# Kernel tuning notes

Measured on AMD Instinct MI355X. Metric: run time of the kernel, lower is better.

The kernel has to match this reference:

```python
import jax, jax.numpy as jnp
import numpy as np

EPS = 1e-12  # torch F.normalize default eps


def _l2norm(t, axis=-1):
    n = jnp.sqrt(jnp.sum(t * t, axis=axis, keepdims=True))
    return t / jnp.maximum(n, EPS)


def setup_inputs() -> dict:
    key = jax.random.key(0)
    ks = jax.random.split(key, 5)
    B, N, C, H = 8, 4096, 1024, 16
    x = jax.random.normal(ks[0], (B, N, C), dtype=jnp.float32)
    # nn.Linear(dim, 3*dim, bias=False): weight [3C, C]; we store transposed [C, 3C]
    w_qkv = jax.random.normal(ks[1], (C, 3 * C), dtype=jnp.float32) * (1.0 / np.sqrt(C))
    temperature = jnp.ones((H, 1, 1), dtype=jnp.float32)
    w_proj = jax.random.normal(ks[2], (C, C), dtype=jnp.float32) * (1.0 / np.sqrt(C))
    b_proj = jax.random.normal(ks[3], (C,), dtype=jnp.float32) * 0.01
    return {"x": x, "w_qkv": w_qkv, "temperature": temperature,
            "w_proj": w_proj, "b_proj": b_proj}


def reference(x, w_qkv, temperature, w_proj, b_proj):
    B, N, C = x.shape
    H = temperature.shape[0]
    dh = C // H
    # qkv: [B, N, 3C] -> [B, N, 3, H, dh] -> q/k/v each [B, H, dh, N]
    qkv = (x @ w_qkv).reshape(B, N, 3, H, dh).transpose(2, 0, 3, 4, 1)
    q, k, v = qkv[0], qkv[1], qkv[2]
    # L2-normalize over token axis (last dim)
    q = _l2norm(q)
    k = _l2norm(k)
    # channel-channel attention: [B, H, dh, dh]
    attn = jnp.einsum("bhdn,bhen->bhde", q, k) * temperature  # temp broadcasts [H,1,1]
    attn = jax.nn.softmax(attn, axis=-1)
    # weighted sum over channels: [B, H, dh, N] -> [B, N, C]
    out = jnp.einsum("bhde,bhen->bhdn", attn, v).transpose(0, 3, 1, 2).reshape(B, N, C)
    return out @ w_proj + b_proj
```

## Files before the change

kernel.cpp:

```cpp
#include <hip/hip_runtime.h>
#include <cstdint>

typedef unsigned short u16;
typedef unsigned int u32;
typedef __attribute__((ext_vector_type(8))) short bf16x8;
typedef __attribute__((ext_vector_type(4))) float f32x4;

typedef const u32 __attribute__((address_space(1)))* gp_t;
typedef u32 __attribute__((address_space(3)))* lp_t;

__device__ __forceinline__ u16 f2bf(float f) {
    union { float f; u32 u; } v; v.f = f;
    u32 r = v.u + 0x7FFFu + ((v.u >> 16) & 1u);
    return (u16)(r >> 16);
}
__device__ __forceinline__ float bf2f(u16 h) {
    union { u32 u; float f; } v; v.u = ((u32)h) << 16;
    return v.f;
}

__global__ __launch_bounds__(256) void k_pack2(const float* __restrict__ x,
                                               u16* __restrict__ xt, u16* __restrict__ xc) {
    __shared__ u16 tb[64][72];
    const int blk = blockIdx.x;
    const int tt = blk >> 4, ct = blk & 15;
    const long tok0 = (long)tt * 64;
    const int ch0 = ct * 64;
    const int tid = threadIdx.x;
    const int row = tid >> 2, cq = tid & 3;
#pragma unroll
    for (int jj = 0; jj < 4; ++jj) {
        const float4 v = *(const float4*)(x + (tok0 + row) * 1024 + ch0 + cq * 16 + jj * 4);
        tb[row][cq * 16 + jj * 4 + 0] = f2bf(v.x);
        tb[row][cq * 16 + jj * 4 + 1] = f2bf(v.y);
        tb[row][cq * 16 + jj * 4 + 2] = f2bf(v.z);
        tb[row][cq * 16 + jj * 4 + 3] = f2bf(v.w);
    }
    __syncthreads();
#pragma unroll
    for (int s = 0; s < 2; ++s) {
        const int c = s * 256 + tid;
        const int r2 = c >> 3, col8 = c & 7;
        *(uint4*)(xt + (tok0 + r2) * 1024 + ch0 + col8 * 8) = *(const uint4*)(&tb[r2][col8 * 8]);
    }
    const int b = (int)(tok0 >> 12);
    const int nin = (int)(tok0 & 4095);
#pragma unroll
    for (int s = 0; s < 2; ++s) {
        const int c = s * 256 + tid;
        const int crow = c >> 3, t8 = c & 7;
        u16 u[8];
#pragma unroll
        for (int k = 0; k < 8; ++k) u[k] = tb[t8 * 8 + k][crow];
        *(uint4*)(xc + ((long)b * 1024 + ch0 + crow) * 4096 + nin + t8 * 8) = *(const uint4*)u;
    }
}

__global__ __launch_bounds__(256) void k_prep(
    const float* __restrict__ wqkv, const float* __restrict__ wproj,
    u16* __restrict__ wqT, u16* __restrict__ wpT, u16* __restrict__ wvb)
{
    __shared__ float t[64][65];
    const int blk = blockIdx.x;
    const int tid = threadIdx.x;
    if (blk < 1024) {
        const float* src; u16* dst; int ncols, lb;
        if (blk < 768) { src = wqkv; dst = wqT; ncols = 3072; lb = blk; }
        else           { src = wproj; dst = wpT; ncols = 1024; lb = blk - 768; }
        const int ntn = ncols >> 6;
        const int kb = (lb / ntn) * 64;
        const int nb = (lb % ntn) * 64;
        for (int i = tid; i < 4096; i += 256) {
            int r = i >> 6, c = i & 63;
            t[r][c] = src[(long)(kb + r) * ncols + nb + c];
        }
        __syncthreads();
        for (int i = tid; i < 4096; i += 256) {
            int r = i >> 6, c = i & 63;
            dst[(long)(nb + r) * 1024 + kb + c] = f2bf(t[c][r]);
        }
    } else {
        const int idx = (blk - 1024) * 256 + tid;
        const int cin = idx >> 7, e0 = (idx & 127) * 8;
        const float4 v1 = *(const float4*)(wqkv + (long)cin * 3072 + 2048 + e0);
        const float4 v2 = *(const float4*)(wqkv + (long)cin * 3072 + 2048 + e0 + 4);
        u16 u[8];
        u[0] = f2bf(v1.x); u[1] = f2bf(v1.y); u[2] = f2bf(v1.z); u[3] = f2bf(v1.w);
        u[4] = f2bf(v2.x); u[5] = f2bf(v2.y); u[6] = f2bf(v2.z); u[7] = f2bf(v2.w);
        *(uint4*)(wvb + (long)cin * 1024 + e0) = *(const uint4*)u;
    }
}

__global__ __launch_bounds__(256) void k_g128p(
    const u16* __restrict__ xc, float* __restrict__ Sp)
{
    __shared__ u16 sm[8192];

    const int tid = threadIdx.x;
    const int wid = tid >> 6, lane = tid & 63;
    const int wr = wid >> 1, wc = wid & 1;
    const int fr = lane & 15, sl = lane >> 4;

    const int nwg = gridDim.x;
    const int logical = (blockIdx.x & 7) * (nwg >> 3) + (blockIdx.x >> 3);
    const int kseg = logical & 3;
    const int bt = logical >> 2;
    const int b = bt / 36;
    int t = bt % 36;
    int i0 = 0;
    while (t >= 8 - i0) { t -= 8 - i0; ++i0; }
    const int j0 = i0 + t;
    const int m0 = i0 * 128, n0 = j0 * 128;

    const u16* base = xc + (long)b * 4194304 + kseg * 1024;

    const int srow = lane >> 2;
    const int sslot = lane & 3;

    f32x4 acc[4][4];
#pragma unroll
    for (int i = 0; i < 4; ++i)
#pragma unroll
        for (int j = 0; j < 4; ++j) acc[i][j] = (f32x4){0.f, 0.f, 0.f, 0.f};

    for (int kt = 0; kt < 1024; kt += 32) {
        __syncthreads();
#pragma unroll
        for (int i = 0; i < 2; ++i) {
            const int row = wid * 32 + i * 16 + srow;
            const int swz = (sslot ^ ((row >> 1) & 3)) << 3;
            const u16* ga = base + (long)(m0 + row) * 4096 + kt + swz;
            const u16* gb = base + (long)(n0 + row) * 4096 + kt + swz;
            __builtin_amdgcn_global_load_lds((gp_t)ga, (lp_t)(sm + (wid * 2 + i) * 512), 16, 0, 0);
            __builtin_amdgcn_global_load_lds((gp_t)gb, (lp_t)(sm + 4096 + (wid * 2 + i) * 512), 16, 0, 0);
        }
        __syncthreads();
        bf16x8 af[4], bfr[4];
#pragma unroll
        for (int mi = 0; mi < 4; ++mi) {
            const int row = wr * 64 + mi * 16 + fr;
            af[mi] = *(const bf16x8*)(sm + row * 32 + ((sl ^ ((row >> 1) & 3)) << 3));
        }
#pragma unroll
        for (int ni = 0; ni < 4; ++ni) {
            const int row = wc * 64 + ni * 16 + fr;
            bfr[ni] = *(const bf16x8*)(sm + 4096 + row * 32 + ((sl ^ ((row >> 1) & 3)) << 3));
        }
#pragma unroll
        for (int mi = 0; mi < 4; ++mi)
#pragma unroll
            for (int ni = 0; ni < 4; ++ni)
                acc[mi][ni] = __builtin_amdgcn_mfma_f32_16x16x32_bf16(af[mi], bfr[ni], acc[mi][ni], 0, 0, 0);
    }

    float* gp = Sp + (long)logical * 16384;
#pragma unroll
    for (int mi = 0; mi < 4; ++mi)
#pragma unroll
        for (int ni = 0; ni < 4; ++ni)
#pragma unroll
            for (int rr = 0; rr < 4; ++rr)
                gp[(wr * 64 + mi * 16 + sl * 4 + rr) * 128 + wc * 64 + ni * 16 + fr] = acc[mi][ni][rr];
}

__global__ __launch_bounds__(256) void k_sred(const float* __restrict__ Sp, u16* __restrict__ S)
{
    __shared__ u16 lC[128 * 136];
    __shared__ u16 lCT[128 * 136];

    const int tid = threadIdx.x;
    const int nwg = gridDim.x;
    const int logical = (blockIdx.x & 7) * (nwg >> 3) + (blockIdx.x >> 3);
    const int b = logical / 36;
    int t = logical % 36;
    int i0 = 0;
    while (t >= 8 - i0) { t -= 8 - i0; ++i0; }
    const int j0 = i0 + t;
    const int m0 = i0 * 128, n0 = j0 * 128;

    const float* p = Sp + (long)logical * 65536;
    for (int i = tid; i < 16384; i += 256) {
        const float s = p[i] + p[i + 16384] + p[i + 32768] + p[i + 49152];
        const u16 v = f2bf(s);
        const int r_ = i >> 7, c_ = i & 127;
        lC[r_ * 136 + c_] = v;
        lCT[c_ * 136 + r_] = v;
    }
    __syncthreads();
    const int tk = tid >> 1, half = tid & 1;
    {
        u16* dp = S + (long)b * 1048576 + (long)(m0 + tk) * 1024 + n0 + half * 64;
        const u16* sp1 = lC + tk * 136 + half * 64;
#pragma unroll
        for (int i = 0; i < 8; ++i) ((uint4*)dp)[i] = ((const uint4*)sp1)[i];
    }
    if (i0 != j0) {
        u16* dp = S + (long)b * 1048576 + (long)(n0 + tk) * 1024 + m0 + half * 64;
        const u16* sp2 = lCT + tk * 136 + half * 64;
#pragma unroll
        for (int i = 0; i < 8; ++i) ((uint4*)dp)[i] = ((const uint4*)sp2)[i];
    }
}

__global__ __launch_bounds__(256) void k_g128(
    const u16* __restrict__ A, long Ab, const u16* __restrict__ Bt, long Bs,
    u16* __restrict__ C, long Cb, int K, int MT, int NT)
{
    __shared__ u16 sm[8192];
    __shared__ u16 lC[128 * 136];

    const int tid = threadIdx.x;
    const int wid = tid >> 6, lane = tid & 63;
    const int wr = wid >> 1, wc = wid & 1;
    const int fr = lane & 15, sl = lane >> 4;

    const int nwg = gridDim.x;
    const int logical = (blockIdx.x & 7) * (nwg >> 3) + (blockIdx.x >> 3);

    const int b = logical / (MT * NT);
    const int r = logical % (MT * NT);
    const int i0 = r / NT, j0 = r % NT;
    const int m0 = i0 * 128, n0 = j0 * 128;
    const u16* Abp = A + (long)b * Ab;
    const u16* Bbp = Bt + (long)b * Bs;
    u16* Cbp = C + (long)b * Cb;

    const int srow = lane >> 2;
    const int sslot = lane & 3;

    f32x4 acc[4][4];
#pragma unroll
    for (int i = 0; i < 4; ++i)
#pragma unroll
        for (int j = 0; j < 4; ++j) acc[i][j] = (f32x4){0.f, 0.f, 0.f, 0.f};

    for (int kt = 0; kt < K; kt += 32) {
        __syncthreads();
#pragma unroll
        for (int i = 0; i < 2; ++i) {
            const int row = wid * 32 + i * 16 + srow;
            const int swz = (sslot ^ ((row >> 1) & 3)) << 3;
            const u16* ga = Abp + (long)(m0 + row) * K + kt + swz;
            const u16* gb = Bbp + (long)(n0 + row) * K + kt + swz;
            __builtin_amdgcn_global_load_lds((gp_t)ga, (lp_t)(sm + (wid * 2 + i) * 512), 16, 0, 0);
            __builtin_amdgcn_global_load_lds((gp_t)gb, (lp_t)(sm + 4096 + (wid * 2 + i) * 512), 16, 0, 0);
        }
        __syncthreads();
        bf16x8 af[4], bfr[4];
#pragma unroll
        for (int mi = 0; mi < 4; ++mi) {
            const int row = wr * 64 + mi * 16 + fr;
            af[mi] = *(const bf16x8*)(sm + row * 32 + ((sl ^ ((row >> 1) & 3)) << 3));
        }
#pragma unroll
        for (int ni = 0; ni < 4; ++ni) {
            const int row = wc * 64 + ni * 16 + fr;
            bfr[ni] = *(const bf16x8*)(sm + 4096 + row * 32 + ((sl ^ ((row >> 1) & 3)) << 3));
        }
#pragma unroll
        for (int mi = 0; mi < 4; ++mi)
#pragma unroll
            for (int ni = 0; ni < 4; ++ni)
                acc[mi][ni] = __builtin_amdgcn_mfma_f32_16x16x32_bf16(af[mi], bfr[ni], acc[mi][ni], 0, 0, 0);
    }
    __syncthreads();

#pragma unroll
    for (int mi = 0; mi < 4; ++mi)
#pragma unroll
        for (int ni = 0; ni < 4; ++ni) {
            const int ch = wc * 64 + ni * 16 + fr;
            const int tk = wr * 64 + mi * 16 + sl * 4;
#pragma unroll
            for (int rr = 0; rr < 4; ++rr)
                lC[(tk + rr) * 136 + ch] = f2bf(acc[mi][ni][rr]);
        }
    __syncthreads();
    {
        const int tk = tid >> 1, half = tid & 1;
        const u16* sp = lC + tk * 136 + half * 64;
        u16* dp = Cbp + (long)(m0 + tk) * 1024 + n0 + half * 64;
#pragma unroll
        for (int i = 0; i < 8; ++i) ((uint4*)dp)[i] = ((const uint4*)sp)[i];
    }
}

template<int EPI>
__global__ __launch_bounds__(512, 2) void k_gemm256(
    const u16* __restrict__ A, long Ab, const u16* __restrict__ Bt, long Bs,
    int MT, int NT,
    u16* __restrict__ cB, float* __restrict__ cF, long Cb, const float* __restrict__ bias)
{
    __shared__ uint4 smem4[8704];
    u16* sm = (u16*)smem4;

    const int tid = threadIdx.x;
    const int wid = tid >> 6, lane = tid & 63;
    const int wr = wid >> 2, wc = wid & 3;
    const int fr = lane & 15, sl = lane >> 4;

    const int nwg = gridDim.x;
    const int logical = (blockIdx.x & 7) * (nwg >> 3) + (blockIdx.x >> 3);
    const int b = logical / (MT * NT);
    const int rem = logical % (MT * NT);
    const int mt = rem / NT, nt = rem % NT;
    const long m0 = (long)mt * 256;
    const int n0 = nt * 256;

    const int srow = wid * 32 + (lane >> 2);
    const int kswz = (((lane & 3) ^ ((srow >> 1) & 3)) << 3);
    const u16* gA = A + (long)b * Ab + (m0 + srow) * 1024L + kswz;
    const u16* gB = Bt + (long)b * Bs + ((long)n0 + srow) * 1024L + kswz;
    const int ldst = wid * 1024;

    const int fxor = ((sl ^ ((fr >> 1) & 3)) << 3);
    const int aBase = (wr * 128 + fr) * 32 + fxor;
    const int bBase = 32768 + (wc * 64 + fr) * 32 + fxor;

    f32x4 acc[8][4];
#pragma unroll
    for (int i = 0; i < 8; ++i)
#pragma unroll
        for (int j = 0; j < 4; ++j) acc[i][j] = (f32x4){0.f, 0.f, 0.f, 0.f};

#define STAGE_A(d, kh, ts) do { \
    const u16* g_ = gA + (ts) * 64 + (kh) * 32; \
    u16* l_ = sm + (d) * 16384 + (kh) * 8192 + ldst; \
    __builtin_amdgcn_global_load_lds((gp_t)g_, (lp_t)l_, 16, 0, 0); \
    __builtin_amdgcn_global_load_lds((gp_t)(g_ + 16 * 1024), (lp_t)(l_ + 512), 16, 0, 0); \
} while (0)
#define STAGE_B(d, kh, ts) do { \
    const u16* g_ = gB + (ts) * 64 + (kh) * 32; \
    u16* l_ = sm + 32768 + (d) * 16384 + (kh) * 8192 + ldst; \
    __builtin_amdgcn_global_load_lds((gp_t)g_, (lp_t)l_, 16, 0, 0); \
    __builtin_amdgcn_global_load_lds((gp_t)(g_ + 16 * 1024), (lp_t)(l_ + 512), 16, 0, 0); \
} while (0)

    STAGE_A(0, 0, 0); STAGE_B(0, 0, 0);
    STAGE_A(0, 1, 0); STAGE_B(0, 1, 0);
    STAGE_A(1, 0, 1); STAGE_B(1, 0, 1);
    asm volatile("s_waitcnt vmcnt(8)" ::: "memory");
    __builtin_amdgcn_s_barrier();

    bf16x8 afX[4], afY[4], bfX[4], bfY[4];
#pragma unroll
    for (int ni = 0; ni < 4; ++ni) bfX[ni] = *(const bf16x8*)(sm + bBase + ni * 512);
#pragma unroll
    for (int mi = 0; mi < 4; ++mi) afX[mi] = *(const bf16x8*)(sm + aBase + mi * 512);

#pragma unroll 2
    for (int T = 0; T < 16; ++T) {
        const int d = T & 1;
        const int t1 = (T + 1 < 16) ? T + 1 : 15;
        const int t2 = (T + 2 < 16) ? T + 2 : 15;
        const int base = d * 16384;
        const int nbase = (d ^ 1) * 16384;

#pragma unroll
        for (int mi = 0; mi < 4; ++mi)
            afY[mi] = *(const bf16x8*)(sm + aBase + (4 + mi) * 512 + base);
        STAGE_A(d ^ 1, 1, t1);
        asm volatile("s_waitcnt vmcnt(6)" ::: "memory");
        __builtin_amdgcn_s_barrier();
        __builtin_amdgcn_s_setprio(1);
#pragma unroll
        for (int mi = 0; mi < 4; ++mi)
#pragma unroll
            for (int ni = 0; ni < 4; ++ni)
                acc[mi][ni] = __builtin_amdgcn_mfma_f32_16x16x32_bf16(afX[mi], bfX[ni], acc[mi][ni], 0, 0, 0);
        __builtin_amdgcn_s_setprio(0);
        __builtin_amdgcn_s_barrier();

#pragma unroll
        for (int ni = 0; ni < 4; ++ni)
            bfY[ni] = *(const bf16x8*)(sm + bBase + ni * 512 + base + 8192);
#pragma unroll
        for (int mi = 0; mi < 4; ++mi)
            afX[mi] = *(const bf16x8*)(sm + aBase + mi * 512 + base + 8192);
        STAGE_B(d ^ 1, 1, t1);
        __builtin_amdgcn_s_barrier();
        __builtin_amdgcn_s_setprio(1);
#pragma unroll
        for (int mi = 0; mi < 4; ++mi)
#pragma unroll
            for (int ni = 0; ni < 4; ++ni)
                acc[mi + 4][ni] = __builtin_amdgcn_mfma_f32_16x16x32_bf16(afY[mi], bfX[ni], acc[mi + 4][ni], 0, 0, 0);
        __builtin_amdgcn_s_setprio(0);
        __builtin_amdgcn_s_barrier();

#pragma unroll
        for (int mi = 0; mi < 4; ++mi)
            afY[mi] = *(const bf16x8*)(sm + aBase + (4 + mi) * 512 + base + 8192);
        STAGE_A(d, 0, t2);
        asm volatile("s_waitcnt vmcnt(6)" ::: "memory");
        __builtin_amdgcn_s_barrier();
        __builtin_amdgcn_s_setprio(1);
#pragma unroll
        for (int mi = 0; mi < 4; ++mi)
#pragma unroll
            for (int ni = 0; ni < 4; ++ni)
                acc[mi][ni] = __builtin_amdgcn_mfma_f32_16x16x32_bf16(afX[mi], bfY[ni], acc[mi][ni], 0, 0, 0);
        __builtin_amdgcn_s_setprio(0);
        __builtin_amdgcn_s_barrier();

#pragma unroll
        for (int ni = 0; ni < 4; ++ni)
            bfX[ni] = *(const bf16x8*)(sm + bBase + ni * 512 + nbase);
#pragma unroll
        for (int mi = 0; mi < 4; ++mi)
            afX[mi] = *(const bf16x8*)(sm + aBase + mi * 512 + nbase);
        STAGE_B(d, 0, t2);
        __builtin_amdgcn_s_barrier();
        __builtin_amdgcn_s_setprio(1);
#pragma unroll
        for (int mi = 0; mi < 4; ++mi)
#pragma unroll
            for (int ni = 0; ni < 4; ++ni)
                acc[mi + 4][ni] = __builtin_amdgcn_mfma_f32_16x16x32_bf16(afY[mi], bfY[ni], acc[mi + 4][ni], 0, 0, 0);
        __builtin_amdgcn_s_setprio(0);
        __builtin_amdgcn_s_barrier();
    }
#undef STAGE_A
#undef STAGE_B
    asm volatile("s_waitcnt vmcnt(0)" ::: "memory");
    __syncthreads();

    if (EPI == 0) {
        u16* cbase = cB + (long)b * Cb;
        u16* piece = sm + wid * 8704;
#pragma unroll
        for (int mi = 0; mi < 8; ++mi)
#pragma unroll
            for (int ni = 0; ni < 4; ++ni) {
                const int ch = ni * 16 + fr;
                const int tk = mi * 16 + sl * 4;
#pragma unroll
                for (int rr = 0; rr < 4; ++rr)
                    piece[(tk + rr) * 68 + ch] = f2bf(acc[mi][ni][rr]);
            }
        __syncthreads();
#pragma unroll
        for (int i = 0; i < 32; ++i) {
            const int chunk = i * 512 + tid;
            const int row = chunk >> 4, c8 = chunk & 15;
            const int p = row >> 7, tk = row & 127;
            const int wrp = p >> 2, wcp = p & 3;
            const uint2 v = *(const uint2*)(sm + p * 8704 + tk * 68 + c8 * 4);
            *(uint2*)(cbase + (m0 + wrp * 128 + tk) * 1024L + n0 + wcp * 64 + c8 * 4) = v;
        }
    } else {
        float* cbase = cF + (long)b * Cb;
        float bi[4];
#pragma unroll
        for (int ni = 0; ni < 4; ++ni) bi[ni] = bias[n0 + wc * 64 + ni * 16 + fr];
#pragma unroll
        for (int pass = 0; pass < 2; ++pass) {
            float* pieceF = (float*)smem4 + wid * 4352;
            if (pass) __syncthreads();
#pragma unroll
            for (int mi2 = 0; mi2 < 4; ++mi2) {
                const int mi = pass * 4 + mi2;
#pragma unroll
                for (int ni = 0; ni < 4; ++ni) {
                    const int ch = ni * 16 + fr;
                    const int tk = mi2 * 16 + sl * 4;
#pragma unroll
                    for (int rr = 0; rr < 4; ++rr)
                        pieceF[(tk + rr) * 68 + ch] = acc[mi][ni][rr] + bi[ni];
                }
            }
            __syncthreads();
#pragma unroll
            for (int i = 0; i < 16; ++i) {
                const int chunk = i * 512 + tid;
                const int row = chunk >> 4, c4 = chunk & 15;
                const int p = row >> 6, tk = row & 63;
                const int wrp = p >> 2, wcp = p & 3;
                const float4 v = *(const float4*)((float*)smem4 + p * 4352 + tk * 68 + c4 * 4);
                *(float4*)(cbase + (m0 + wrp * 128 + pass * 64 + tk) * 1024L + n0 + wcp * 64 + c4 * 4) = v;
            }
        }
    }
}

__global__ __launch_bounds__(256) void k_gram2p(
    const u16* __restrict__ wqT, const u16* __restrict__ Ut,
    float* __restrict__ g2p, float* __restrict__ sq2p)
{
    __shared__ u16 lQ[64 * 256];
    __shared__ u16 lK[64 * 256];

    const int blk = blockIdx.x;
    const int seg = blk & 3, bh = blk >> 2;
    const int b = bh >> 4, h = bh & 15;
    const int tid = threadIdx.x;
    const int wid = tid >> 6, lane = tid & 63;

    {
        const int r2 = lane >> 5, slot = lane & 31;
        const int rbase = wid * 16;
#pragma unroll
        for (int i = 0; i < 8; ++i) {
            const int r = rbase + i * 2 + r2;
            const int col = seg * 256 + ((slot ^ (r & 7)) << 3);
            const u16* gq = wqT + (long)(h * 64 + r) * 1024 + col;
            const u16* gk = Ut + ((long)b * 2048 + 1024 + h * 64 + r) * 1024 + col;
            __builtin_amdgcn_global_load_lds((gp_t)gq, (lp_t)(lQ + (rbase + i * 2) * 256), 16, 0, 0);
            __builtin_amdgcn_global_load_lds((gp_t)gk, (lp_t)(lK + (rbase + i * 2) * 256), 16, 0, 0);
        }
    }
    __syncthreads();

    {
        const int row = tid >> 1, half = tid & 1;
        const int j = (row < 64) ? (h * 64 + row) : (1024 + h * 64 + (row - 64));
        const u16* pa = wqT + (long)j * 1024 + seg * 256 + half * 128;
        const u16* pb = Ut + ((long)b * 2048 + j) * 1024 + seg * 256 + half * 128;
        float s = 0.f;
#pragma unroll 4
        for (int i = 0; i < 16; ++i) {
            const uint4 a = *(const uint4*)(pa + i * 8);
            const uint4 bv = *(const uint4*)(pb + i * 8);
            s += bf2f((u16)(a.x & 0xFFFF)) * bf2f((u16)(bv.x & 0xFFFF));
            s += bf2f((u16)(a.x >> 16))    * bf2f((u16)(bv.x >> 16));
            s += bf2f((u16)(a.y & 0xFFFF)) * bf2f((u16)(bv.y & 0xFFFF));
            s += bf2f((u16)(a.y >> 16))    * bf2f((u16)(bv.y >> 16));
            s += bf2f((u16)(a.z & 0xFFFF)) * bf2f((u16)(bv.z & 0xFFFF));
            s += bf2f((u16)(a.z >> 16))    * bf2f((u16)(bv.z >> 16));
            s += bf2f((u16)(a.w & 0xFFFF)) * bf2f((u16)(bv.w & 0xFFFF));
            s += bf2f((u16)(a.w >> 16))    * bf2f((u16)(bv.w >> 16));
        }
        s += __shfl_xor(s, 1);
        if (half == 0) sq2p[(long)blk * 128 + row] = s;
    }

    const int fr = lane & 15, sl = lane >> 4;
    f32x4 acc[4];
#pragma unroll
    for (int i = 0; i < 4; ++i) acc[i] = (f32x4){0.f, 0.f, 0.f, 0.f};
#pragma unroll
    for (int ks = 0; ks < 8; ++ks) {
        const int ra = wid * 16 + fr;
        const bf16x8 a = *(const bf16x8*)(lQ + ra * 256 + (((ks * 4 + sl) ^ (ra & 7)) << 3));
#pragma unroll
        for (int ni = 0; ni < 4; ++ni) {
            const int rb = ni * 16 + fr;
            const bf16x8 bb = *(const bf16x8*)(lK + rb * 256 + (((ks * 4 + sl) ^ (rb & 7)) << 3));
            acc[ni] = __builtin_amdgcn_mfma_f32_16x16x32_bf16(a, bb, acc[ni], 0, 0, 0);
        }
    }
    float* gp = g2p + (long)blk * 4096;
#pragma unroll
    for (int ni = 0; ni < 4; ++ni)
#pragma unroll
        for (int rr = 0; rr < 4; ++rr)
            gp[(wid * 16 + sl * 4 + rr) * 64 + ni * 16 + fr] = acc[ni][rr];
}

__global__ __launch_bounds__(256) void k_swmix(
    const float* __restrict__ g2p, const float* __restrict__ sq2p,
    const float* __restrict__ temperature,
    const u16* __restrict__ wpT, u16* __restrict__ wmix)
{
    __shared__ u16 lA[64 * 72];
    __shared__ u16 lB[256 * 64];

    const int blk = blockIdx.x;
    const int nseg = blk & 3, bh = blk >> 2;
    const int b = bh >> 4, h = bh & 15;
    const int tid = threadIdx.x;
    const int wid = tid >> 6, lane = tid & 63;
    const int fr = lane & 15, sl = lane >> 4;

#pragma unroll
    for (int i = 0; i < 8; ++i) {
        const int cc = wid * 8 + i;
        const int row = cc * 8 + (lane >> 3);
        const int slot = lane & 7;
        const u16* g = wpT + (long)(nseg * 256 + row) * 1024 + h * 64 + ((slot ^ (row & 7)) << 3);
        __builtin_amdgcn_global_load_lds((gp_t)g, (lp_t)(lB + cc * 512), 16, 0, 0);
    }

    {
        const int e = lane;
        const float* sp = sq2p + (long)bh * 512;
        float sqk = 0.f;
#pragma unroll
        for (int s = 0; s < 4; ++s) sqk += sp[s * 128 + 64 + e];
        const float rk = 1.f / fmaxf(sqrtf(sqk), 1e-12f);
        const float temp = temperature[h];
        const float* gp = g2p + (long)bh * 16384;
#pragma unroll 2
        for (int i = 0; i < 16; ++i) {
            const int d = wid * 16 + i;
            float raw = 0.f, sqq = 0.f;
#pragma unroll
            for (int s = 0; s < 4; ++s) {
                raw += gp[s * 4096 + d * 64 + e];
                sqq += sp[s * 128 + d];
            }
            const float rq = 1.f / fmaxf(sqrtf(sqq), 1e-12f);
            const float v = raw * rq * rk * temp;
            float mx = v;
#pragma unroll
            for (int o = 32; o; o >>= 1) mx = fmaxf(mx, __shfl_xor(mx, o));
            const float p = __expf(v - mx);
            float sum = p;
#pragma unroll
            for (int o = 32; o; o >>= 1) sum += __shfl_xor(sum, o);
            lA[e * 72 + d] = f2bf(p / sum);
        }
    }
    __syncthreads();

    f32x4 acc[4][4];
#pragma unroll
    for (int i = 0; i < 4; ++i)
#pragma unroll
        for (int j = 0; j < 4; ++j) acc[i][j] = (f32x4){0.f, 0.f, 0.f, 0.f};

#pragma unroll
    for (int ks = 0; ks < 2; ++ks) {
        bf16x8 a[4], bb[4];
#pragma unroll
        for (int mi = 0; mi < 4; ++mi)
            a[mi] = *(const bf16x8*)(lA + (mi * 16 + fr) * 72 + ks * 32 + sl * 8);
#pragma unroll
        for (int ni = 0; ni < 4; ++ni) {
            const int rb = wid * 64 + ni * 16 + fr;
            bb[ni] = *(const bf16x8*)(lB + rb * 64 + (((ks * 4 + sl) ^ (rb & 7)) << 3));
        }
#pragma unroll
        for (int mi = 0; mi < 4; ++mi)
#pragma unroll
            for (int ni = 0; ni < 4; ++ni)
                acc[mi][ni] = __builtin_amdgcn_mfma_f32_16x16x32_bf16(a[mi], bb[ni], acc[mi][ni], 0, 0, 0);
    }

    u16* dst = wmix + ((long)b << 20);
#pragma unroll
    for (int mi = 0; mi < 4; ++mi)
#pragma unroll
        for (int ni = 0; ni < 4; ++ni) {
            const int cout = nseg * 256 + wid * 64 + ni * 16 + fr;
            const int e0 = mi * 16 + sl * 4;
            ushort4 w;
            w.x = f2bf(acc[mi][ni][0]); w.y = f2bf(acc[mi][ni][1]);
            w.z = f2bf(acc[mi][ni][2]); w.w = f2bf(acc[mi][ni][3]);
            *(ushort4*)(dst + (long)cout * 1024 + h * 64 + e0) = w;
        }
}

extern "C" void kernel_launch(void* const* d_in, const int* in_sizes, int n_in,
                              void* d_out, int out_size, void* d_ws, size_t ws_size,
                              hipStream_t stream) {
    const float* x = (const float*)d_in[0];
    const float* w_qkv = (const float*)d_in[1];
    const float* temperature = (const float*)d_in[2];
    const float* w_proj = (const float*)d_in[3];
    const float* b_proj = (const float*)d_in[4];
    float* out = (float*)d_out;
    char* ws = (char*)d_ws;

    u16* wqT    = (u16*)(ws);
    u16* wpT    = (u16*)(ws + 6291456);
    u16* wvb    = (u16*)(ws + 8388608);
    u16* xt     = (u16*)(ws + 10485760);
    u16* xc     = (u16*)(ws + 77594624);
    u16* S      = (u16*)(ws + 144703488);
    float* Sp   = (float*)(ws + 161480704);
    u16* Ut     = (u16*)(ws + 161480704);
    float* g2p  = (float*)(ws + 195035136);
    float* sq2p = (float*)(ws + 203423744);
    u16* wmix   = (u16*)(ws + 204734464);
    u16* wfinT  = (u16*)(ws + 221511680);

    k_pack2<<<8192, 256, 0, stream>>>(x, xt, xc);
    k_prep<<<1536, 256, 0, stream>>>(w_qkv, w_proj, wqT, wpT, wvb);
    k_g128p<<<1152, 256, 0, stream>>>(xc, Sp);
    k_sred<<<288, 256, 0, stream>>>(Sp, S);
    k_gemm256<0><<<256, 512, 0, stream>>>(wqT, 0L, S, 1048576L, 8, 4, Ut, nullptr, 2097152L, nullptr);
    k_gram2p<<<512, 256, 0, stream>>>(wqT, Ut, g2p, sq2p);
    k_swmix<<<512, 256, 0, stream>>>(g2p, sq2p, temperature, wpT, wmix);
    k_g128<<<512, 256, 0, stream>>>(wmix, 1048576L, wvb, 0L, wfinT, 1048576L, 1024, 8, 8);
    k_gemm256<1><<<512, 512, 0, stream>>>(xt, 4194304L, wfinT, 1048576L, 16, 4, nullptr, out, 4194304L, b_proj);
}
```

Before: 345.3 us.

## Merge pack and prep kernels, halve Gram split-K, store partials as bf16

The x pack/transposition kernel and the weight prep kernel are merged into one launch with block-range dispatch. The Gram split-K goes from 4 segments to 2 (576 blocks, each doing twice the K loop), and partial results are written as bf16 instead of fp32. The reduction kernel reads the bf16 halves with vectorised loads. This cuts partial-sum traffic and one launch, at the cost of fewer blocks for the Gram GEMM (under-occupancy risk) and extra rounding of the partials.

```diff
diff --git a/kernel.cpp b/kernel.cpp
--- a/kernel.cpp
+++ b/kernel.cpp
@@ -19,68 +19,66 @@
     return v.f;
 }
 
-__global__ __launch_bounds__(256) void k_pack2(const float* __restrict__ x,
-                                               u16* __restrict__ xt, u16* __restrict__ xc) {
-    __shared__ u16 tb[64][72];
-    const int blk = blockIdx.x;
-    const int tt = blk >> 4, ct = blk & 15;
-    const long tok0 = (long)tt * 64;
-    const int ch0 = ct * 64;
-    const int tid = threadIdx.x;
-    const int row = tid >> 2, cq = tid & 3;
-#pragma unroll
-    for (int jj = 0; jj < 4; ++jj) {
-        const float4 v = *(const float4*)(x + (tok0 + row) * 1024 + ch0 + cq * 16 + jj * 4);
-        tb[row][cq * 16 + jj * 4 + 0] = f2bf(v.x);
-        tb[row][cq * 16 + jj * 4 + 1] = f2bf(v.y);
-        tb[row][cq * 16 + jj * 4 + 2] = f2bf(v.z);
-        tb[row][cq * 16 + jj * 4 + 3] = f2bf(v.w);
-    }
-    __syncthreads();
-#pragma unroll
-    for (int s = 0; s < 2; ++s) {
-        const int c = s * 256 + tid;
-        const int r2 = c >> 3, col8 = c & 7;
-        *(uint4*)(xt + (tok0 + r2) * 1024 + ch0 + col8 * 8) = *(const uint4*)(&tb[r2][col8 * 8]);
-    }
-    const int b = (int)(tok0 >> 12);
-    const int nin = (int)(tok0 & 4095);
-#pragma unroll
-    for (int s = 0; s < 2; ++s) {
-        const int c = s * 256 + tid;
-        const int crow = c >> 3, t8 = c & 7;
-        u16 u[8];
-#pragma unroll
-        for (int k = 0; k < 8; ++k) u[k] = tb[t8 * 8 + k][crow];
-        *(uint4*)(xc + ((long)b * 1024 + ch0 + crow) * 4096 + nin + t8 * 8) = *(const uint4*)u;
-    }
-}
-
-__global__ __launch_bounds__(256) void k_prep(
-    const float* __restrict__ wqkv, const float* __restrict__ wproj,
+__global__ __launch_bounds__(256) void k_prepack(
+    const float* __restrict__ x, const float* __restrict__ wqkv, const float* __restrict__ wproj,
+    u16* __restrict__ xt, u16* __restrict__ xc,
     u16* __restrict__ wqT, u16* __restrict__ wpT, u16* __restrict__ wvb)
 {
-    __shared__ float t[64][65];
+    __shared__ float tf[64][65];
     const int blk = blockIdx.x;
     const int tid = threadIdx.x;
-    if (blk < 1024) {
+
+    if (blk < 8192) {
+        u16* tb = (u16*)tf;
+        const int tt = blk >> 4, ct = blk & 15;
+        const long tok0 = (long)tt * 64;
+        const int ch0 = ct * 64;
+        const int row = tid >> 2, cq = tid & 3;
+#pragma unroll
+        for (int jj = 0; jj < 4; ++jj) {
+            const float4 v = *(const float4*)(x + (tok0 + row) * 1024 + ch0 + cq * 16 + jj * 4);
+            tb[row * 72 + cq * 16 + jj * 4 + 0] = f2bf(v.x);
+            tb[row * 72 + cq * 16 + jj * 4 + 1] = f2bf(v.y);
+            tb[row * 72 + cq * 16 + jj * 4 + 2] = f2bf(v.z);
+            tb[row * 72 + cq * 16 + jj * 4 + 3] = f2bf(v.w);
+        }
+        __syncthreads();
+#pragma unroll
+        for (int s = 0; s < 2; ++s) {
+            const int c = s * 256 + tid;
+            const int r2 = c >> 3, col8 = c & 7;
+            *(uint4*)(xt + (tok0 + r2) * 1024 + ch0 + col8 * 8) = *(const uint4*)(&tb[r2 * 72 + col8 * 8]);
+        }
+        const int b = (int)(tok0 >> 12);
+        const int nin = (int)(tok0 & 4095);
+#pragma unroll
+        for (int s = 0; s < 2; ++s) {
+            const int c = s * 256 + tid;
+            const int crow = c >> 3, t8 = c & 7;
+            u16 u[8];
+#pragma unroll
+            for (int k = 0; k < 8; ++k) u[k] = tb[(t8 * 8 + k) * 72 + crow];
+            *(uint4*)(xc + ((long)b * 1024 + ch0 + crow) * 4096 + nin + t8 * 8) = *(const uint4*)u;
+        }
+    } else if (blk < 9216) {
+        const int lb0 = blk - 8192;
         const float* src; u16* dst; int ncols, lb;
-        if (blk < 768) { src = wqkv; dst = wqT; ncols = 3072; lb = blk; }
-        else           { src = wproj; dst = wpT; ncols = 1024; lb = blk - 768; }
+        if (lb0 < 768) { src = wqkv; dst = wqT; ncols = 3072; lb = lb0; }
+        else           { src = wproj; dst = wpT; ncols = 1024; lb = lb0 - 768; }
         const int ntn = ncols >> 6;
         const int kb = (lb / ntn) * 64;
         const int nb = (lb % ntn) * 64;
         for (int i = tid; i < 4096; i += 256) {
             int r = i >> 6, c = i & 63;
-            t[r][c] = src[(long)(kb + r) * ncols + nb + c];
+            tf[r][c] = src[(long)(kb + r) * ncols + nb + c];
         }
         __syncthreads();
         for (int i = tid; i < 4096; i += 256) {
             int r = i >> 6, c = i & 63;
-            dst[(long)(nb + r) * 1024 + kb + c] = f2bf(t[c][r]);
+            dst[(long)(nb + r) * 1024 + kb + c] = f2bf(tf[c][r]);
         }
     } else {
-        const int idx = (blk - 1024) * 256 + tid;
+        const int idx = (blk - 9216) * 256 + tid;
         const int cin = idx >> 7, e0 = (idx & 127) * 8;
         const float4 v1 = *(const float4*)(wqkv + (long)cin * 3072 + 2048 + e0);
         const float4 v2 = *(const float4*)(wqkv + (long)cin * 3072 + 2048 + e0 + 4);
@@ -92,7 +90,7 @@
 }
 
 __global__ __launch_bounds__(256) void k_g128p(
-    const u16* __restrict__ xc, float* __restrict__ Sp)
+    const u16* __restrict__ xc, u16* __restrict__ Spb)
 {
     __shared__ u16 sm[8192];
 
@@ -103,8 +101,8 @@
 
     const int nwg = gridDim.x;
     const int logical = (blockIdx.x & 7) * (nwg >> 3) + (blockIdx.x >> 3);
-    const int kseg = logical & 3;
-    const int bt = logical >> 2;
+    const int kseg = logical & 1;
+    const int bt = logical >> 1;
     const int b = bt / 36;
     int t = bt % 36;
     int i0 = 0;
@@ -112,7 +110,7 @@
     const int j0 = i0 + t;
     const int m0 = i0 * 128, n0 = j0 * 128;
 
-    const u16* base = xc + (long)b * 4194304 + kseg * 1024;
+    const u16* base = xc + (long)b * 4194304 + kseg * 2048;
 
     const int srow = lane >> 2;
     const int sslot = lane & 3;
@@ -123,7 +121,7 @@
 #pragma unroll
         for (int j = 0; j < 4; ++j) acc[i][j] = (f32x4){0.f, 0.f, 0.f, 0.f};
 
-    for (int kt = 0; kt < 1024; kt += 32) {
+    for (int kt = 0; kt < 2048; kt += 32) {
         __syncthreads();
 #pragma unroll
         for (int i = 0; i < 2; ++i) {
@@ -153,17 +151,20 @@
                 acc[mi][ni] = __builtin_amdgcn_mfma_f32_16x16x32_bf16(af[mi], bfr[ni], acc[mi][ni], 0, 0, 0);
     }
 
-    float* gp = Sp + (long)logical * 16384;
+    u16* gp = Spb + (long)logical * 16384;
 #pragma unroll
     for (int mi = 0; mi < 4; ++mi)
 #pragma unroll
-        for (int ni = 0; ni < 4; ++ni)
+        for (int ni = 0; ni < 4; ++ni) {
+            const int rw = wr * 64 + mi * 16 + sl * 4;
+            const int cl = wc * 64 + ni * 16 + fr;
 #pragma unroll
             for (int rr = 0; rr < 4; ++rr)
-                gp[(wr * 64 + mi * 16 + sl * 4 + rr) * 128 + wc * 64 + ni * 16 + fr] = acc[mi][ni][rr];
-}
-
-__global__ __launch_bounds__(256) void k_sred(const float* __restrict__ Sp, u16* __restrict__ S)
+                gp[(rw + rr) * 128 + cl] = f2bf(acc[mi][ni][rr]);
+        }
+}
+
+__global__ __launch_bounds__(256) void k_sred(const u16* __restrict__ Spb, u16* __restrict__ S)
 {
     __shared__ u16 lC[128 * 136];
     __shared__ u16 lCT[128 * 136];
@@ -178,13 +179,23 @@
     const int j0 = i0 + t;
     const int m0 = i0 * 128, n0 = j0 * 128;
 
-    const float* p = Sp + (long)logical * 65536;
-    for (int i = tid; i < 16384; i += 256) {
-        const float s = p[i] + p[i + 16384] + p[i + 32768] + p[i + 49152];
-        const u16 v = f2bf(s);
-        const int r_ = i >> 7, c_ = i & 127;
-        lC[r_ * 136 + c_] = v;
-        lCT[c_ * 136 + r_] = v;
+    const u16* p = Spb + (long)logical * 32768;
+    for (int c8 = tid; c8 < 2048; c8 += 256) {
+        const uint4 a = *(const uint4*)(p + c8 * 8);
+        const uint4 b2 = *(const uint4*)(p + 16384 + c8 * 8);
+        u16 o[8];
+        o[0] = f2bf(bf2f((u16)(a.x & 0xFFFF)) + bf2f((u16)(b2.x & 0xFFFF)));
+        o[1] = f2bf(bf2f((u16)(a.x >> 16))    + bf2f((u16)(b2.x >> 16)));
+        o[2] = f2bf(bf2f((u16)(a.y & 0xFFFF)) + bf2f((u16)(b2.y & 0xFFFF)));
+        o[3] = f2bf(bf2f((u16)(a.y >> 16))    + bf2f((u16)(b2.y >> 16)));
+        o[4] = f2bf(bf2f((u16)(a.z & 0xFFFF)) + bf2f((u16)(b2.z & 0xFFFF)));
+        o[5] = f2bf(bf2f((u16)(a.z >> 16))    + bf2f((u16)(b2.z >> 16)));
+        o[6] = f2bf(bf2f((u16)(a.w & 0xFFFF)) + bf2f((u16)(b2.w & 0xFFFF)));
+        o[7] = f2bf(bf2f((u16)(a.w >> 16))    + bf2f((u16)(b2.w >> 16)));
+        const int r_ = c8 >> 4, c0 = (c8 & 15) * 8;
+        *(uint4*)(lC + r_ * 136 + c0) = *(const uint4*)o;
+#pragma unroll
+        for (int k = 0; k < 8; ++k) lCT[(c0 + k) * 136 + r_] = o[k];
     }
     __syncthreads();
     const int tk = tid >> 1, half = tid & 1;
@@ -668,17 +679,16 @@
     u16* xt     = (u16*)(ws + 10485760);
     u16* xc     = (u16*)(ws + 77594624);
     u16* S      = (u16*)(ws + 144703488);
-    float* Sp   = (float*)(ws + 161480704);
+    u16* Spb    = (u16*)(ws + 161480704);
     u16* Ut     = (u16*)(ws + 161480704);
     float* g2p  = (float*)(ws + 195035136);
     float* sq2p = (float*)(ws + 203423744);
     u16* wmix   = (u16*)(ws + 204734464);
     u16* wfinT  = (u16*)(ws + 221511680);
 
-    k_pack2<<<8192, 256, 0, stream>>>(x, xt, xc);
-    k_prep<<<1536, 256, 0, stream>>>(w_qkv, w_proj, wqT, wpT, wvb);
-    k_g128p<<<1152, 256, 0, stream>>>(xc, Sp);
-    k_sred<<<288, 256, 0, stream>>>(Sp, S);
+    k_prepack<<<9728, 256, 0, stream>>>(x, w_qkv, w_proj, xt, xc, wqT, wpT, wvb);
+    k_g128p<<<576, 256, 0, stream>>>(xc, Spb);
+    k_sred<<<288, 256, 0, stream>>>(Spb, S);
     k_gemm256<0><<<256, 512, 0, stream>>>(wqT, 0L, S, 1048576L, 8, 4, Ut, nullptr, 2097152L, nullptr);
     k_gram2p<<<512, 256, 0, stream>>>(wqT, Ut, g2p, sq2p);
     k_swmix<<<512, 256, 0, stream>>>(g2p, sq2p, temperature, wpT, wmix);
```

Measured after the change: 317.0 us. 8.2% less time.
